# Performance work log

Measured on AMD Instinct MI355X. Metric: run time of the kernel, lower is better.

## Reference

```python
import jax, jax.numpy as jnp
import numpy as np

N = 16384   # 32 graphs x 512 nodes
E_RAND = 500000
H, C, D, F, L = 4, 64, 256, 1024, 4  # heads, head_dim, model dim, ffn dim, layers


def setup_inputs() -> dict:
    key = jax.random.key(0)
    ks = jax.random.split(key, 8)
    ei = jax.random.randint(ks[0], (2, E_RAND), 0, N)
    loops = jnp.arange(N)
    edge_index = jnp.concatenate([ei, jnp.stack([loops, loops])], axis=1)  # add_self_loops
    s = 0.05
    return dict(
        hf=jax.random.normal(ks[1], (N, D), dtype=jnp.float32),
        hs=jax.random.normal(ks[2], (N, D), dtype=jnp.float32),
        edge_index=edge_index,
        Wgat=jax.random.normal(ks[3], (2, L, D, D), dtype=jnp.float32) * s,
        att_src=jax.random.normal(ks[4], (2, L, H, C), dtype=jnp.float32) * s,
        att_dst=jax.random.normal(ks[5], (2, L, H, C), dtype=jnp.float32) * s,
        bias_gat=jnp.zeros((2, L, D), dtype=jnp.float32),
        W1=jax.random.normal(ks[6], (2, L, D, F), dtype=jnp.float32) * s,
        b1=jnp.zeros((2, L, F), dtype=jnp.float32),
        W2=jax.random.normal(ks[7], (2, L, F, D), dtype=jnp.float32) * s,
        b2=jnp.zeros((2, L, D), dtype=jnp.float32),
        g1=jnp.ones((2, L, D), dtype=jnp.float32),
        bt1=jnp.zeros((2, L, D), dtype=jnp.float32),
        g2=jnp.ones((2, L, D), dtype=jnp.float32),
        bt2=jnp.zeros((2, L, D), dtype=jnp.float32),
    )


def _ln(x, g, b):
    m = jnp.mean(x, -1, keepdims=True)
    v = jnp.var(x, -1, keepdims=True)
    return (x - m) * jax.lax.rsqrt(v + 1e-5) * g + b


def _gat_encoder_layer(x, src, dst, Wg, asr, ads, bg, W1, b1, W2, b2, g1, bt1, g2, bt2):
    # GATConv (PyG semantics): linear proj, per-edge attention, segment softmax over dst
    h = (x @ Wg).reshape(N, H, C)                       # [N,H,C]
    a_s = (h * asr).sum(-1)                             # [N,H]
    a_d = (h * ads).sum(-1)                             # [N,H]
    e = jax.nn.leaky_relu(a_s[src] + a_d[dst], 0.2)     # [E,H]
    m = jax.ops.segment_max(e, dst, num_segments=N)
    ex = jnp.exp(e - m[dst])
    den = jax.ops.segment_sum(ex, dst, num_segments=N)
    alpha = ex / jnp.maximum(den[dst], 1e-16)           # [E,H]
    agg = jax.ops.segment_sum(h[src] * alpha[:, :, None], dst, num_segments=N)
    out = agg.reshape(N, H * C) + bg                    # concat heads + bias
    # residual + norm1 (dropout=0.0)
    x1 = _ln(out + x, g1, bt1)
    # FFN + residual + norm2
    f = jax.nn.relu(x1 @ W1 + b1) @ W2 + b2
    return _ln(f + x1, g2, bt2)


def reference(hf, hs, edge_index, Wgat, att_src, att_dst, bias_gat, W1, b1, W2, b2, g1, bt1, g2, bt2):
    src, dst = edge_index[0], edge_index[1]
    for i in range(L):
        hf_new = _gat_encoder_layer(hf + hs, src, dst, Wgat[0, i], att_src[0, i], att_dst[0, i],
                                    bias_gat[0, i], W1[0, i], b1[0, i], W2[0, i], b2[0, i],
                                    g1[0, i], bt1[0, i], g2[0, i], bt2[0, i])
        hs = _gat_encoder_layer(hs, src, dst, Wgat[1, i], att_src[1, i], att_dst[1, i],
                                bias_gat[1, i], W1[1, i], b1[1, i], W2[1, i], b2[1, i],
                                g1[1, i], bt1[1, i], g2[1, i], bt2[1, i])
        hf = hf_new
    return (hf, hs)
```

## Files before the change

### kernel.cpp

```cpp
#include <hip/hip_runtime.h>

#define Nn 16384
#define Dm 256
#define Ff 1024

typedef __attribute__((ext_vector_type(8))) short bf16x8;
typedef __attribute__((ext_vector_type(4))) float f32x4;

typedef const __attribute__((address_space(1))) unsigned int glb_u32;
typedef __attribute__((address_space(3))) unsigned int lds_u32;

__device__ __forceinline__ void async_copy16(const void* g, void* l) {
  __builtin_amdgcn_global_load_lds((glb_u32*)g, (lds_u32*)l, 16, 0, 0);
}

__device__ __forceinline__ unsigned short f2bf(float f) {
  union { float f; unsigned u; } v; v.f = f;
  return (unsigned short)((v.u + 0x7FFFu + ((v.u >> 16) & 1u)) >> 16);
}

__device__ __forceinline__ float bf2f(unsigned short u) {
  union { unsigned u; float f; } v; v.u = ((unsigned)u) << 16;
  return v.f;
}

__device__ __forceinline__ float sel4(float4 v, int h) {
  float r = v.x;
  r = (h == 1) ? v.y : r;
  r = (h == 2) ? v.z : r;
  r = (h == 3) ? v.w : r;
  return r;
}

__global__ __launch_bounds__(256) void wconvt_kernel(const float* __restrict__ w,
                                                     unsigned short* __restrict__ wt,
                                                     int K, int J) {
  __shared__ unsigned short t[64][65];
  int b = blockIdx.z;
  int j0 = blockIdx.x * 64, k0 = blockIdx.y * 64;
  int tj = threadIdx.x & 63, q = threadIdx.x >> 6;
  const float* wb = w + (size_t)b * K * J;
#pragma unroll
  for (int r = 0; r < 16; ++r) {
    int k = r * 4 + q;
    t[k][tj] = f2bf(wb[(size_t)(k0 + k) * J + j0 + tj]);
  }
  __syncthreads();
  unsigned short* wtb = wt + (size_t)b * K * J;
#pragma unroll
  for (int r = 0; r < 16; ++r) {
    int j = r * 4 + q;
    wtb[(size_t)(j0 + j) * K + k0 + tj] = t[tj][j];
  }
}

__global__ void count_kernel(const int* __restrict__ dst, int E, int* __restrict__ cnt) {
  for (int e = blockIdx.x * blockDim.x + threadIdx.x; e < E; e += gridDim.x * blockDim.x)
    atomicAdd(&cnt[dst[e]], 1);
}

__global__ __launch_bounds__(256) void scan1_kernel(const int* __restrict__ cnt,
                                                    int* __restrict__ part,
                                                    int* __restrict__ bsum) {
  __shared__ int sd[256];
  int b = blockIdx.x, tid = threadIdx.x;
  int v = cnt[b * 256 + tid];
  sd[tid] = v;
  __syncthreads();
  for (int offt = 1; offt < 256; offt <<= 1) {
    int t = (tid >= offt) ? sd[tid - offt] : 0;
    __syncthreads();
    sd[tid] += t;
    __syncthreads();
  }
  part[b * 256 + tid] = sd[tid] - v;
  if (tid == 255) bsum[b] = sd[255];
}

__global__ __launch_bounds__(64) void scan2_kernel(const int* __restrict__ bsum,
                                                   int* __restrict__ bbase,
                                                   int* __restrict__ rowptr) {
  __shared__ int sd[64];
  int tid = threadIdx.x;
  int v = bsum[tid];
  sd[tid] = v;
  __syncthreads();
  for (int offt = 1; offt < 64; offt <<= 1) {
    int t = (tid >= offt) ? sd[tid - offt] : 0;
    __syncthreads();
    sd[tid] += t;
    __syncthreads();
  }
  bbase[tid] = sd[tid] - v;
  if (tid == 63) rowptr[Nn] = sd[63];
}

__global__ __launch_bounds__(256) void scan3_kernel(const int* __restrict__ part,
                                                    const int* __restrict__ bbase,
                                                    int* __restrict__ rowptr,
                                                    int* __restrict__ cursor) {
  int b = blockIdx.x, tid = threadIdx.x;
  int v = part[b * 256 + tid] + bbase[b];
  rowptr[b * 256 + tid] = v;
  cursor[b * 256 + tid] = v;
}

__global__ void fill_kernel(const int* __restrict__ src, const int* __restrict__ dst, int E,
                            int* __restrict__ cursor, int* __restrict__ csrc) {
  for (int e = blockIdx.x * blockDim.x + threadIdx.x; e < E; e += gridDim.x * blockDim.x) {
    int pos = atomicAdd(&cursor[dst[e]], 1);
    csrc[pos] = src[e];
  }
}

__global__ void prep_kernel(const float* __restrict__ hf, const float* __restrict__ hs,
                            unsigned short* __restrict__ x01b, int total) {
  const size_t ZS = (size_t)Nn * Dm;
  for (int i = blockIdx.x * blockDim.x + threadIdx.x; i < total; i += gridDim.x * blockDim.x) {
    float a = hf[i], b = hs[i];
    x01b[i] = f2bf(a + b);
    x01b[ZS + i] = f2bf(b);
  }
}

__global__ __launch_bounds__(256, 2) void proj_kernel(
    const unsigned short* __restrict__ xib, const unsigned short* __restrict__ Wgt_l,
    unsigned short* __restrict__ hbuf2, const float* __restrict__ asr_l,
    const float* __restrict__ ads_l, float* __restrict__ a_s2, float* __restrict__ a_d2) {
  __shared__ __align__(16) unsigned short sA[128 * 64];
  __shared__ __align__(16) unsigned short sB[64 * 64];
  const int K = 256;
  const size_t ZS = (size_t)Nn * Dm;
  int tid = threadIdx.x;
  int wave = tid >> 6, lane = tid & 63;
  int l16 = lane & 15, lhi = lane >> 4;
  int brow = blockIdx.x, bcol = blockIdx.y, z = blockIdx.z;
  int wm = wave >> 1, wn = wave & 1;

  const unsigned short* Ab = xib + z * ZS + (size_t)brow * 128 * K;
  const unsigned short* Bb = Wgt_l + (size_t)z * 4 * 65536 + (size_t)bcol * 64 * K;
  int lrow = lane >> 3, lk = (lane & 7) * 8;

  f32x4 acc[4][2] = {};

  for (int k0 = 0; k0 < K; k0 += 64) {
#pragma unroll
    for (int r = 0; r < 4; ++r) {
      int rb = r * 32 + wave * 8;
      async_copy16(Ab + (size_t)(rb + lrow) * K + k0 + lk, &sA[rb * 64]);
      if (r < 2)
        async_copy16(Bb + (size_t)(rb + lrow) * K + k0 + lk, &sB[rb * 64]);
    }
    __syncthreads();
#pragma unroll
    for (int kk = 0; kk < 2; ++kk) {
      bf16x8 af[4], bfr[2];
#pragma unroll
      for (int mi = 0; mi < 4; ++mi)
        af[mi] = *(const bf16x8*)&sA[(wm * 64 + mi * 16 + l16) * 64 + kk * 32 + lhi * 8];
#pragma unroll
      for (int ni = 0; ni < 2; ++ni)
        bfr[ni] = *(const bf16x8*)&sB[(wn * 32 + ni * 16 + l16) * 64 + kk * 32 + lhi * 8];
#pragma unroll
      for (int mi = 0; mi < 4; ++mi)
#pragma unroll
        for (int ni = 0; ni < 2; ++ni)
          acc[mi][ni] = __builtin_amdgcn_mfma_f32_16x16x32_bf16(af[mi], bfr[ni], acc[mi][ni], 0, 0, 0);
    }
    __syncthreads();
  }

  unsigned short* hb = hbuf2 + z * ZS;
  const float* asr_p = asr_l + z * 1024 + bcol * 64;
  const float* ads_p = ads_l + z * 1024 + bcol * 64;
  float as0 = asr_p[wn * 32 + l16],      ad0 = ads_p[wn * 32 + l16];
  float as1 = asr_p[wn * 32 + 16 + l16], ad1 = ads_p[wn * 32 + 16 + l16];
  float* sredS = (float*)sA;
  float* sredD = (float*)sA + 256;

#pragma unroll
  for (int mi = 0; mi < 4; ++mi) {
#pragma unroll
    for (int j = 0; j < 4; ++j) {
      int r = brow * 128 + wm * 64 + mi * 16 + lhi * 4 + j;
      float v0 = acc[mi][0][j], v1 = acc[mi][1][j];
      hb[(size_t)r * 256 + bcol * 64 + wn * 32 + l16] = f2bf(v0);
      hb[(size_t)r * 256 + bcol * 64 + wn * 32 + 16 + l16] = f2bf(v1);
      float ps = v0 * as0 + v1 * as1;
      float pd = v0 * ad0 + v1 * ad1;
#pragma unroll
      for (int off = 1; off < 16; off <<= 1) {
        ps += __shfl_xor(ps, off);
        pd += __shfl_xor(pd, off);
      }
      if (l16 == 0) {
        int rl = mi * 16 + lhi * 4 + j;
        sredS[wm * 128 + wn * 64 + rl] = ps;
        sredD[wm * 128 + wn * 64 + rl] = pd;
      }
    }
  }
  __syncthreads();
  if (tid < 128) {
    int w = tid >> 6, rl = tid & 63;
    float s = sredS[w * 128 + rl] + sredS[w * 128 + 64 + rl];
    float d = sredD[w * 128 + rl] + sredD[w * 128 + 64 + rl];
    int row = brow * 128 + tid;
    a_s2[(size_t)z * Nn * 4 + row * 4 + bcol] = s;
    a_d2[(size_t)z * Nn * 4 + row * 4 + bcol] = d;
  }
}

__global__ __launch_bounds__(256, 2) void ffn1_kernel(
    const unsigned short* __restrict__ A2, const unsigned short* __restrict__ Bt_l,
    unsigned short* __restrict__ out2, const float* __restrict__ b1_l) {
  const int K = 256, Ncol = Ff;
  const size_t ZS = (size_t)Nn * Dm;
  __shared__ __align__(16) unsigned short sA[128 * 64];
  __shared__ __align__(16) unsigned short sB[128 * 64];
  int tid = threadIdx.x, wave = tid >> 6, lane = tid & 63;
  int l16 = lane & 15, lhi = lane >> 4;
  int brow = blockIdx.x, bcol = blockIdx.y, z = blockIdx.z;
  int wm = wave >> 1, wn = wave & 1;

  const unsigned short* Ab = A2 + z * ZS + (size_t)brow * 128 * K;
  const unsigned short* Bb = Bt_l + (size_t)z * 4 * Ff * 256 + (size_t)bcol * 128 * K;
  int lrow = lane >> 3, lk = (lane & 7) * 8;

  f32x4 acc[4][4] = {};

  for (int k0 = 0; k0 < K; k0 += 64) {
#pragma unroll
    for (int r = 0; r < 4; ++r) {
      int rb = r * 32 + wave * 8;
      async_copy16(Ab + (size_t)(rb + lrow) * K + k0 + lk, &sA[rb * 64]);
      async_copy16(Bb + (size_t)(rb + lrow) * K + k0 + lk, &sB[rb * 64]);
    }
    __syncthreads();
#pragma unroll
    for (int kk = 0; kk < 2; ++kk) {
      bf16x8 af[4], bfr[4];
#pragma unroll
      for (int mi = 0; mi < 4; ++mi)
        af[mi] = *(const bf16x8*)&sA[(wm * 64 + mi * 16 + l16) * 64 + kk * 32 + lhi * 8];
#pragma unroll
      for (int ni = 0; ni < 4; ++ni)
        bfr[ni] = *(const bf16x8*)&sB[(wn * 64 + ni * 16 + l16) * 64 + kk * 32 + lhi * 8];
#pragma unroll
      for (int mi = 0; mi < 4; ++mi)
#pragma unroll
        for (int ni = 0; ni < 4; ++ni)
          acc[mi][ni] = __builtin_amdgcn_mfma_f32_16x16x32_bf16(af[mi], bfr[ni], acc[mi][ni], 0, 0, 0);
    }
    __syncthreads();
  }

  unsigned short* outB = out2 + (size_t)z * Nn * Ff;
  const float* bias = b1_l + z * 4096;
#pragma unroll
  for (int mi = 0; mi < 4; ++mi) {
#pragma unroll
    for (int ni = 0; ni < 4; ++ni) {
#pragma unroll
      for (int j = 0; j < 4; ++j) {
        int r = brow * 128 + wm * 64 + mi * 16 + lhi * 4 + j;
        int c = bcol * 128 + wn * 64 + ni * 16 + l16;
        float v = acc[mi][ni][j] + bias[c];
        v = v > 0.f ? v : 0.f;
        outB[(size_t)r * Ncol + c] = f2bf(v);
      }
    }
  }
}

__global__ __launch_bounds__(256, 2) void ffn2_kernel(
    const unsigned short* __restrict__ A2, const unsigned short* __restrict__ Bt_l,
    unsigned short* __restrict__ out2, const float* __restrict__ b2_l,
    const unsigned short* __restrict__ resid2) {
  const int K = Ff, Ncol = 256;
  const size_t ZS = (size_t)Nn * Dm;
  __shared__ __align__(16) unsigned short sA[128 * 64];
  __shared__ __align__(16) unsigned short sB[64 * 64];
  int tid = threadIdx.x, wave = tid >> 6, lane = tid & 63;
  int l16 = lane & 15, lhi = lane >> 4;
  int brow = blockIdx.x, bcol = blockIdx.y, z = blockIdx.z;
  int wm = wave >> 1, wn = wave & 1;

  const unsigned short* Ab = A2 + (size_t)z * Nn * Ff + (size_t)brow * 128 * K;
  const unsigned short* Bb = Bt_l + (size_t)z * 4 * Ff * 256 + (size_t)bcol * 64 * K;
  int lrow = lane >> 3, lk = (lane & 7) * 8;

  f32x4 acc[4][2] = {};

  for (int k0 = 0; k0 < K; k0 += 64) {
#pragma unroll
    for (int r = 0; r < 4; ++r) {
      int rb = r * 32 + wave * 8;
      async_copy16(Ab + (size_t)(rb + lrow) * K + k0 + lk, &sA[rb * 64]);
      if (r < 2)
        async_copy16(Bb + (size_t)(rb + lrow) * K + k0 + lk, &sB[rb * 64]);
    }
    __syncthreads();
#pragma unroll
    for (int kk = 0; kk < 2; ++kk) {
      bf16x8 af[4], bfr[2];
#pragma unroll
      for (int mi = 0; mi < 4; ++mi)
        af[mi] = *(const bf16x8*)&sA[(wm * 64 + mi * 16 + l16) * 64 + kk * 32 + lhi * 8];
#pragma unroll
      for (int ni = 0; ni < 2; ++ni)
        bfr[ni] = *(const bf16x8*)&sB[(wn * 32 + ni * 16 + l16) * 64 + kk * 32 + lhi * 8];
#pragma unroll
      for (int mi = 0; mi < 4; ++mi)
#pragma unroll
        for (int ni = 0; ni < 2; ++ni)
          acc[mi][ni] = __builtin_amdgcn_mfma_f32_16x16x32_bf16(af[mi], bfr[ni], acc[mi][ni], 0, 0, 0);
    }
    __syncthreads();
  }

  unsigned short* outB = out2 + z * ZS;
  const float* bias = b2_l + z * 1024;
  const unsigned short* resid = resid2 + z * ZS;
#pragma unroll
  for (int mi = 0; mi < 4; ++mi) {
#pragma unroll
    for (int ni = 0; ni < 2; ++ni) {
#pragma unroll
      for (int j = 0; j < 4; ++j) {
        int r = brow * 128 + wm * 64 + mi * 16 + lhi * 4 + j;
        int c = bcol * 64 + wn * 32 + ni * 16 + l16;
        float v = acc[mi][ni][j] + bias[c] + bf2f(resid[(size_t)r * Ncol + c]);
        outB[(size_t)r * Ncol + c] = f2bf(v);
      }
    }
  }
}

__global__ __launch_bounds__(256) void agg_kernel(
    const unsigned short* __restrict__ hbuf2, const float* __restrict__ a_s2,
    const float* __restrict__ a_d2,
    const int* __restrict__ rowptr, const int* __restrict__ csrc,
    const float* __restrict__ bias_l, const unsigned short* __restrict__ x01b,
    const float* __restrict__ g1_l, const float* __restrict__ bt1_l,
    unsigned short* __restrict__ x1b2) {
  __shared__ float sw[4][320];
  __shared__ int ssrc[4][64];
  const size_t ZS = (size_t)Nn * Dm;
  int z = blockIdx.y;
  const unsigned short* hb = hbuf2 + z * ZS;
  const float* a_s = a_s2 + (size_t)z * Nn * 4;
  const float* a_d = a_d2 + (size_t)z * Nn * 4;
  const float* bias = bias_l + z * 1024;
  const unsigned short* xres = x01b + z * ZS;
  const float* g1 = g1_l + z * 1024;
  const float* bt1 = bt1_l + z * 1024;
  unsigned short* x1b = x1b2 + z * ZS;

  int wave = threadIdx.x >> 6, lane = threadIdx.x & 63;
  int n = blockIdx.x * 4 + wave;
  int l32 = lane & 31;
  int par = lane >> 5;
  int hch = l32 >> 3;
  int c0 = l32 * 8;
  int beg = rowptr[n], end = rowptr[n + 1];
  float4 adv = *(const float4*)&a_d[n * 4];
  const float NI = -__builtin_inff();
  float4 m4 = {NI, NI, NI, NI};
  float acc[8] = {};
  float den = 0.f;

  for (int base = beg; base < end; base += 64) {
    int cnt = min(64, end - base);
    float4 ev = {NI, NI, NI, NI};
    if (lane < cnt) {
      int s = csrc[base + lane];
      ssrc[wave][lane] = s;
      float4 as = *(const float4*)&a_s[s * 4];
      float e0 = as.x + adv.x; ev.x = e0 > 0.f ? e0 : 0.2f * e0;
      float e1 = as.y + adv.y; ev.y = e1 > 0.f ? e1 : 0.2f * e1;
      float e2 = as.z + adv.z; ev.z = e2 > 0.f ? e2 : 0.2f * e2;
      float e3 = as.w + adv.w; ev.w = e3 > 0.f ? e3 : 0.2f * e3;
    }
    float4 mv = ev;
#pragma unroll
    for (int off = 32; off; off >>= 1) {
      mv.x = fmaxf(mv.x, __shfl_xor(mv.x, off));
      mv.y = fmaxf(mv.y, __shfl_xor(mv.y, off));
      mv.z = fmaxf(mv.z, __shfl_xor(mv.z, off));
      mv.w = fmaxf(mv.w, __shfl_xor(mv.w, off));
    }
    float4 m4n;
    m4n.x = fmaxf(m4.x, mv.x); m4n.y = fmaxf(m4.y, mv.y);
    m4n.z = fmaxf(m4.z, mv.z); m4n.w = fmaxf(m4.w, mv.w);
    float rm = __expf(sel4(m4, hch) - sel4(m4n, hch));
#pragma unroll
    for (int j = 0; j < 8; ++j) acc[j] *= rm;
    den *= rm;
    if (lane < cnt) {
      float* swl = &sw[wave][lane * 5];
      swl[0] = __expf(ev.x - m4n.x);
      swl[1] = __expf(ev.y - m4n.y);
      swl[2] = __expf(ev.z - m4n.z);
      swl[3] = __expf(ev.w - m4n.w);
    }
    m4 = m4n;
    __builtin_amdgcn_wave_barrier();
    for (int i = par; i < cnt; i += 2) {
      float w = sw[wave][i * 5 + hch];
      int s_i = ssrc[wave][i];
      bf16x8 hv = *(const bf16x8*)(hb + (size_t)s_i * 256 + c0);
#pragma unroll
      for (int j = 0; j < 8; ++j)
        acc[j] = fmaf(bf2f((unsigned short)hv[j]), w, acc[j]);
      den += w;
    }
    __builtin_amdgcn_wave_barrier();
  }

#pragma unroll
  for (int j = 0; j < 8; ++j) acc[j] += __shfl_xor(acc[j], 32);
  den += __shfl_xor(den, 32);

  float invden = 1.f / fmaxf(den, 1e-16f);
  bf16x8 rv = *(const bf16x8*)(xres + (size_t)n * 256 + c0);
  float outv[8];
  float s1 = 0.f, s2 = 0.f;
#pragma unroll
  for (int j = 0; j < 8; ++j) {
    float v = acc[j] * invden + bias[c0 + j] + bf2f((unsigned short)rv[j]);
    outv[j] = v;
    s1 += v;
    s2 += v * v;
  }
#pragma unroll
  for (int off = 16; off; off >>= 1) {
    s1 += __shfl_xor(s1, off);
    s2 += __shfl_xor(s2, off);
  }
  float mean = s1 * (1.f / 256.f);
  float var = s2 * (1.f / 256.f) - mean * mean;
  float rst = rsqrtf(var + 1e-5f);
  if (par == 0) {
    unsigned short yb[8];
#pragma unroll
    for (int j = 0; j < 8; ++j)
      yb[j] = f2bf((outv[j] - mean) * rst * g1[c0 + j] + bt1[c0 + j]);
    *(bf16x8*)&x1b[(size_t)n * 256 + c0] = *(bf16x8*)yb;
  }
}

template <int PREP>
__global__ __launch_bounds__(256) void ln2_kernel(const unsigned short* __restrict__ tb2,
                                                  const float* __restrict__ g2_l,
                                                  const float* __restrict__ bt2_l,
                                                  float* __restrict__ out_hf,
                                                  float* __restrict__ out_hs,
                                                  unsigned short* __restrict__ x01b) {
  const size_t ZS = (size_t)Nn * Dm;
  int wave = threadIdx.x >> 6, lane = threadIdx.x & 63;
  int n = blockIdx.x * 4 + wave;
  int c0 = lane * 4;
  size_t idx = (size_t)n * 256 + c0;
  ushort4 u0 = *(const ushort4*)&tb2[idx];
  ushort4 u1 = *(const ushort4*)&tb2[ZS + idx];
  float v0[4] = {bf2f(u0.x), bf2f(u0.y), bf2f(u0.z), bf2f(u0.w)};
  float v1[4] = {bf2f(u1.x), bf2f(u1.y), bf2f(u1.z), bf2f(u1.w)};
  float a0 = 0.f, b0 = 0.f, a1 = 0.f, b1 = 0.f;
#pragma unroll
  for (int j = 0; j < 4; ++j) {
    a0 += v0[j]; b0 += v0[j] * v0[j];
    a1 += v1[j]; b1 += v1[j] * v1[j];
  }
#pragma unroll
  for (int off = 32; off; off >>= 1) {
    a0 += __shfl_xor(a0, off);
    b0 += __shfl_xor(b0, off);
    a1 += __shfl_xor(a1, off);
    b1 += __shfl_xor(b1, off);
  }
  float m0 = a0 * (1.f / 256.f), m1 = a1 * (1.f / 256.f);
  float r0 = rsqrtf(b0 * (1.f / 256.f) - m0 * m0 + 1e-5f);
  float r1 = rsqrtf(b1 * (1.f / 256.f) - m1 * m1 + 1e-5f);
  float4 y0, y1;
  unsigned short p0[4], p1[4];
#pragma unroll
  for (int j = 0; j < 4; ++j) {
    float yf = (v0[j] - m0) * r0 * g2_l[c0 + j] + bt2_l[c0 + j];
    float ys = (v1[j] - m1) * r1 * g2_l[1024 + c0 + j] + bt2_l[1024 + c0 + j];
    ((float*)&y0)[j] = yf;
    ((float*)&y1)[j] = ys;
    if (PREP) { p0[j] = f2bf(yf + ys); p1[j] = f2bf(ys); }
  }
  *(float4*)&out_hf[idx] = y0;
  *(float4*)&out_hs[idx] = y1;
  if (PREP) {
    *(ushort4*)&x01b[idx] = *(ushort4*)p0;
    *(ushort4*)&x01b[ZS + idx] = *(ushort4*)p1;
  }
}

extern "C" void kernel_launch(void* const* d_in, const int* in_sizes, int n_in,
                              void* d_out, int out_size, void* d_ws, size_t ws_size,
                              hipStream_t stream) {
  const float* hf_in = (const float*)d_in[0];
  const float* hs_in = (const float*)d_in[1];
  const int* ei = (const int*)d_in[2];
  const int E = in_sizes[2] / 2;
  const float* Wgat = (const float*)d_in[3];
  const float* att_src = (const float*)d_in[4];
  const float* att_dst = (const float*)d_in[5];
  const float* bias_gat = (const float*)d_in[6];
  const float* W1 = (const float*)d_in[7];
  const float* b1 = (const float*)d_in[8];
  const float* W2 = (const float*)d_in[9];
  const float* b2 = (const float*)d_in[10];
  const float* g1 = (const float*)d_in[11];
  const float* bt1 = (const float*)d_in[12];
  const float* g2 = (const float*)d_in[13];
  const float* bt2 = (const float*)d_in[14];
  const int* src = ei;
  const int* dst = ei + E;
  const size_t ZS = (size_t)Nn * Dm;

  char* wsp = (char*)d_ws;
  size_t off = 0;
  auto carve = [&](size_t bytes) -> void* {
    void* p = wsp + off;
    off += (bytes + 255) & ~(size_t)255;
    return p;
  };
  unsigned short* Wgt  = (unsigned short*)carve((size_t)8 * 256 * 256 * 2);
  unsigned short* W1t  = (unsigned short*)carve((size_t)8 * 256 * 1024 * 2);
  unsigned short* W2t  = (unsigned short*)carve((size_t)8 * 1024 * 256 * 2);
  int* cnt      = (int*)carve((size_t)Nn * 4);
  int* rowptr   = (int*)carve((size_t)(Nn + 1) * 4);
  int* cursor   = (int*)carve((size_t)Nn * 4);
  int* part     = (int*)carve((size_t)Nn * 4);
  int* bsum     = (int*)carve((size_t)64 * 4);
  int* bbase    = (int*)carve((size_t)64 * 4);
  int* csrc     = (int*)carve((size_t)E * 4);
  unsigned short* x01b = (unsigned short*)carve(2 * ZS * 2);
  unsigned short* hbuf2 = (unsigned short*)carve(2 * ZS * 2);
  float* a_s2   = (float*)carve((size_t)2 * Nn * 4 * 4);
  float* a_d2   = (float*)carve((size_t)2 * Nn * 4 * 4);
  unsigned short* x1b2 = (unsigned short*)carve(2 * ZS * 2);
  unsigned short* tb2  = (unsigned short*)carve(2 * ZS * 2);
  unsigned short* f_b2 = (unsigned short*)carve((size_t)2 * Nn * Ff * 2);
  if (off > ws_size) return;

  wconvt_kernel<<<dim3(4, 4, 8), 256, 0, stream>>>(Wgat, Wgt, 256, 256);
  wconvt_kernel<<<dim3(16, 4, 8), 256, 0, stream>>>(W1, W1t, 256, 1024);
  wconvt_kernel<<<dim3(4, 16, 8), 256, 0, stream>>>(W2, W2t, 1024, 256);
  hipMemsetAsync(cnt, 0, (size_t)Nn * 4, stream);
  count_kernel<<<1024, 256, 0, stream>>>(dst, E, cnt);
  scan1_kernel<<<64, 256, 0, stream>>>(cnt, part, bsum);
  scan2_kernel<<<1, 64, 0, stream>>>(bsum, bbase, rowptr);
  scan3_kernel<<<64, 256, 0, stream>>>(part, bbase, rowptr, cursor);
  fill_kernel<<<1024, 256, 0, stream>>>(src, dst, E, cursor, csrc);

  float* out_hf = (float*)d_out;
  float* out_hs = out_hf + ZS;

  prep_kernel<<<2048, 256, 0, stream>>>(hf_in, hs_in, x01b, Nn * Dm);

  for (int l = 0; l < 4; ++l) {
    proj_kernel<<<dim3(128, 4, 2), 256, 0, stream>>>(
        x01b, Wgt + (size_t)l * 65536, hbuf2,
        att_src + l * 256, att_dst + l * 256, a_s2, a_d2);
    agg_kernel<<<dim3(Nn / 4, 2), 256, 0, stream>>>(
        hbuf2, a_s2, a_d2, rowptr, csrc,
        bias_gat + l * 256, x01b, g1 + l * 256, bt1 + l * 256, x1b2);
    ffn1_kernel<<<dim3(128, 8, 2), 256, 0, stream>>>(
        x1b2, W1t + (size_t)l * 256 * 1024, f_b2, b1 + l * 1024);
    ffn2_kernel<<<dim3(128, 4, 2), 256, 0, stream>>>(
        f_b2, W2t + (size_t)l * 1024 * 256, tb2, b2 + l * 256, x1b2);
    if (l < 3) {
      ln2_kernel<1><<<Nn / 4, 256, 0, stream>>>(tb2, g2 + l * 256, bt2 + l * 256,
                                                out_hf, out_hs, x01b);
    } else {
      ln2_kernel<0><<<Nn / 4, 256, 0, stream>>>(tb2, g2 + l * 256, bt2 + l * 256,
                                                out_hf, out_hs, x01b);
    }
  }
}
```

Before: 659.0 us.

## Raise GEMM occupancy bounds, add single-chunk softmax fast path, split agg launches

Raises the minimum-blocks hint in the launch bounds of the three GEMM kernels from 2 to 3, pushing the compiler to cap registers so more blocks fit per CU. Adds a fast path in the aggregation kernel for nodes with at most 64 incoming edges that skips the online-softmax rescaling. Splits the two-stream aggregation grid into two separate launches that take the stream index as an argument. Tighter register caps risk spills in the GEMMs, and the extra launch adds overhead.

```diff
diff --git a/kernel.cpp b/kernel.cpp
--- a/kernel.cpp
+++ b/kernel.cpp
@@ -123,7 +123,7 @@
   }
 }
 
-__global__ __launch_bounds__(256, 2) void proj_kernel(
+__global__ __launch_bounds__(256, 3) void proj_kernel(
     const unsigned short* __restrict__ xib, const unsigned short* __restrict__ Wgt_l,
     unsigned short* __restrict__ hbuf2, const float* __restrict__ asr_l,
     const float* __restrict__ ads_l, float* __restrict__ a_s2, float* __restrict__ a_d2) {
@@ -211,7 +211,7 @@
   }
 }
 
-__global__ __launch_bounds__(256, 2) void ffn1_kernel(
+__global__ __launch_bounds__(256, 3) void ffn1_kernel(
     const unsigned short* __restrict__ A2, const unsigned short* __restrict__ Bt_l,
     unsigned short* __restrict__ out2, const float* __restrict__ b1_l) {
   const int K = 256, Ncol = Ff;
@@ -273,7 +273,7 @@
   }
 }
 
-__global__ __launch_bounds__(256, 2) void ffn2_kernel(
+__global__ __launch_bounds__(256, 3) void ffn2_kernel(
     const unsigned short* __restrict__ A2, const unsigned short* __restrict__ Bt_l,
     unsigned short* __restrict__ out2, const float* __restrict__ b2_l,
     const unsigned short* __restrict__ resid2) {
@@ -343,11 +343,10 @@
     const int* __restrict__ rowptr, const int* __restrict__ csrc,
     const float* __restrict__ bias_l, const unsigned short* __restrict__ x01b,
     const float* __restrict__ g1_l, const float* __restrict__ bt1_l,
-    unsigned short* __restrict__ x1b2) {
+    unsigned short* __restrict__ x1b2, int z) {
   __shared__ float sw[4][320];
   __shared__ int ssrc[4][64];
   const size_t ZS = (size_t)Nn * Dm;
-  int z = blockIdx.y;
   const unsigned short* hb = hbuf2 + z * ZS;
   const float* a_s = a_s2 + (size_t)z * Nn * 4;
   const float* a_d = a_d2 + (size_t)z * Nn * 4;
@@ -366,15 +365,14 @@
   int beg = rowptr[n], end = rowptr[n + 1];
   float4 adv = *(const float4*)&a_d[n * 4];
   const float NI = -__builtin_inff();
-  float4 m4 = {NI, NI, NI, NI};
   float acc[8] = {};
   float den = 0.f;
 
-  for (int base = beg; base < end; base += 64) {
-    int cnt = min(64, end - base);
+  if (end - beg <= 64) {
+    int cnt = end - beg;
     float4 ev = {NI, NI, NI, NI};
     if (lane < cnt) {
-      int s = csrc[base + lane];
+      int s = csrc[beg + lane];
       ssrc[wave][lane] = s;
       float4 as = *(const float4*)&a_s[s * 4];
       float e0 = as.x + adv.x; ev.x = e0 > 0.f ? e0 : 0.2f * e0;
@@ -390,21 +388,13 @@
       mv.z = fmaxf(mv.z, __shfl_xor(mv.z, off));
       mv.w = fmaxf(mv.w, __shfl_xor(mv.w, off));
     }
-    float4 m4n;
-    m4n.x = fmaxf(m4.x, mv.x); m4n.y = fmaxf(m4.y, mv.y);
-    m4n.z = fmaxf(m4.z, mv.z); m4n.w = fmaxf(m4.w, mv.w);
-    float rm = __expf(sel4(m4, hch) - sel4(m4n, hch));
-#pragma unroll
-    for (int j = 0; j < 8; ++j) acc[j] *= rm;
-    den *= rm;
     if (lane < cnt) {
       float* swl = &sw[wave][lane * 5];
-      swl[0] = __expf(ev.x - m4n.x);
-      swl[1] = __expf(ev.y - m4n.y);
-      swl[2] = __expf(ev.z - m4n.z);
-      swl[3] = __expf(ev.w - m4n.w);
-    }
-    m4 = m4n;
+      swl[0] = __expf(ev.x - mv.x);
+      swl[1] = __expf(ev.y - mv.y);
+      swl[2] = __expf(ev.z - mv.z);
+      swl[3] = __expf(ev.w - mv.w);
+    }
     __builtin_amdgcn_wave_barrier();
     for (int i = par; i < cnt; i += 2) {
       float w = sw[wave][i * 5 + hch];
@@ -415,7 +405,55 @@
         acc[j] = fmaf(bf2f((unsigned short)hv[j]), w, acc[j]);
       den += w;
     }
-    __builtin_amdgcn_wave_barrier();
+  } else {
+    float4 m4 = {NI, NI, NI, NI};
+    for (int base = beg; base < end; base += 64) {
+      int cnt = min(64, end - base);
+      float4 ev = {NI, NI, NI, NI};
+      if (lane < cnt) {
+        int s = csrc[base + lane];
+        ssrc[wave][lane] = s;
+        float4 as = *(const float4*)&a_s[s * 4];
+        float e0 = as.x + adv.x; ev.x = e0 > 0.f ? e0 : 0.2f * e0;
+        float e1 = as.y + adv.y; ev.y = e1 > 0.f ? e1 : 0.2f * e1;
+        float e2 = as.z + adv.z; ev.z = e2 > 0.f ? e2 : 0.2f * e2;
+        float e3 = as.w + adv.w; ev.w = e3 > 0.f ? e3 : 0.2f * e3;
+      }
+      float4 mv = ev;
+#pragma unroll
+      for (int off = 32; off; off >>= 1) {
+        mv.x = fmaxf(mv.x, __shfl_xor(mv.x, off));
+        mv.y = fmaxf(mv.y, __shfl_xor(mv.y, off));
+        mv.z = fmaxf(mv.z, __shfl_xor(mv.z, off));
+        mv.w = fmaxf(mv.w, __shfl_xor(mv.w, off));
+      }
+      float4 m4n;
+      m4n.x = fmaxf(m4.x, mv.x); m4n.y = fmaxf(m4.y, mv.y);
+      m4n.z = fmaxf(m4.z, mv.z); m4n.w = fmaxf(m4.w, mv.w);
+      float rm = __expf(sel4(m4, hch) - sel4(m4n, hch));
+#pragma unroll
+      for (int j = 0; j < 8; ++j) acc[j] *= rm;
+      den *= rm;
+      if (lane < cnt) {
+        float* swl = &sw[wave][lane * 5];
+        swl[0] = __expf(ev.x - m4n.x);
+        swl[1] = __expf(ev.y - m4n.y);
+        swl[2] = __expf(ev.z - m4n.z);
+        swl[3] = __expf(ev.w - m4n.w);
+      }
+      m4 = m4n;
+      __builtin_amdgcn_wave_barrier();
+      for (int i = par; i < cnt; i += 2) {
+        float w = sw[wave][i * 5 + hch];
+        int s_i = ssrc[wave][i];
+        bf16x8 hv = *(const bf16x8*)(hb + (size_t)s_i * 256 + c0);
+#pragma unroll
+        for (int j = 0; j < 8; ++j)
+          acc[j] = fmaf(bf2f((unsigned short)hv[j]), w, acc[j]);
+        den += w;
+      }
+      __builtin_amdgcn_wave_barrier();
+    }
   }
 
 #pragma unroll
@@ -568,9 +606,12 @@
     proj_kernel<<<dim3(128, 4, 2), 256, 0, stream>>>(
         x01b, Wgt + (size_t)l * 65536, hbuf2,
         att_src + l * 256, att_dst + l * 256, a_s2, a_d2);
-    agg_kernel<<<dim3(Nn / 4, 2), 256, 0, stream>>>(
+    agg_kernel<<<Nn / 4, 256, 0, stream>>>(
         hbuf2, a_s2, a_d2, rowptr, csrc,
-        bias_gat + l * 256, x01b, g1 + l * 256, bt1 + l * 256, x1b2);
+        bias_gat + l * 256, x01b, g1 + l * 256, bt1 + l * 256, x1b2, 0);
+    agg_kernel<<<Nn / 4, 256, 0, stream>>>(
+        hbuf2, a_s2, a_d2, rowptr, csrc,
+        bias_gat + l * 256, x01b, g1 + l * 256, bt1 + l * 256, x1b2, 1);
     ffn1_kernel<<<dim3(128, 8, 2), 256, 0, stream>>>(
         x1b2, W1t + (size_t)l * 256 * 1024, f_b2, b1 + l * 1024);
     ffn2_kernel<<<dim3(128, 4, 2), 256, 0, stream>>>(
```

Result: slower. 681.2 us (+3.4%).
